# Performance work log

Hardware: AMD Instinct MI355X
Metric: run time of the kernel (lower is better)

The kernel has to match this reference:

```python
import jax, jax.numpy as jnp
import numpy as np

EPS = 1e-12  # F.normalize default eps


def setup_inputs() -> dict:
    key = jax.random.key(0)
    k1, k2, k3, k4 = jax.random.split(key, 4)
    b, n, c, h = 8, 4096, 768, 8
    scale = 1.0 / np.sqrt(c)
    return {
        "x": jax.random.normal(k1, (b, n, c), dtype=jnp.float32),
        "W_qkv": jax.random.normal(k2, (c, 3 * c), dtype=jnp.float32) * scale,
        "W_proj": jax.random.normal(k3, (c, c), dtype=jnp.float32) * scale,
        "b_proj": jax.random.normal(k4, (c,), dtype=jnp.float32) * 0.01,
        "temperature": jnp.ones((h, 1, 1), dtype=jnp.float32),
    }


def _l2norm(t):
    # F.normalize(t, dim=-1): t / max(||t||_2, eps)
    nrm = jnp.sqrt(jnp.sum(t * t, axis=-1, keepdims=True))
    return t / jnp.maximum(nrm, EPS)


def reference(x, W_qkv, W_proj, b_proj, temperature):
    b, n, c = x.shape
    h = temperature.shape[0]
    d = c // h  # head_dim
    # qkv: (b, n, 3c) -> (b, n, 3, h, d) -> (3, b, h, d, n)
    qkv = (x @ W_qkv).reshape(b, n, 3, h, d).transpose(2, 0, 3, 4, 1)
    q, k, v = qkv[0], qkv[1], qkv[2]  # each (b, h, d, n)
    qn = _l2norm(q)
    kn = _l2norm(k)
    # cross-covariance attention: (b, h, d, d)
    attn = jnp.einsum('bhdn,bhen->bhde', qn, kn) * temperature
    attn = jax.nn.softmax(attn, axis=-1)
    out = jnp.einsum('bhde,bhen->bhdn', attn, v)  # (b, h, d, n)
    out = out.transpose(0, 3, 1, 2).reshape(b, n, c)
    return out @ W_proj + b_proj
```

## Files before the change

kernel.cpp:

```cpp
#include <hip/hip_runtime.h>
#include <math.h>

#define NB  8
#define SEQ 4096
#define CH  768
#define NH  8
#define HD  96
#define NC3 2304

typedef _Float16 f16x8 __attribute__((ext_vector_type(8)));
typedef float    f32x4 __attribute__((ext_vector_type(4)));

static const size_t XT_B   = 0;
static const size_t UT_B   = 0;
static const size_t ATT_B  = 28311552;
static const size_t MT_B   = 29491200;
static const size_t PT_B   = 38928384;
static const size_t GP_B   = 50331648;
static const size_t XH_B   = 50331648;
static const size_t WH_B   = 100663296;
static const size_t WT_B   = 104202240;
static const size_t WPT_B  = 107741184;
static const size_t G_B    = 108920832;
static const size_t INV_B  = 118358016;
static const size_t XH2_B  = 118407168;
static const size_t XH_BYTES = (size_t)NB * SEQ * CH * 2;

__device__ __forceinline__ void gload16(const void* g, void* l) {
  __builtin_amdgcn_global_load_lds(
      (const __attribute__((address_space(1))) void*)g,
      (__attribute__((address_space(3))) void*)l, 16, 0, 0);
}

__global__ void cvt_f16_kernel(const float* __restrict__ in,
                               _Float16* __restrict__ out, int n4) {
  int i = blockIdx.x * blockDim.x + threadIdx.x;
  if (i < n4) {
    float4 v = *(const float4*)(in + (size_t)i * 4);
    _Float16* o = out + (size_t)i * 4;
    o[0] = (_Float16)v.x; o[1] = (_Float16)v.y;
    o[2] = (_Float16)v.z; o[3] = (_Float16)v.w;
  }
}

__global__ void transpose_cvt_kernel(const float* __restrict__ in,
                                     _Float16* __restrict__ outT,
                                     _Float16* __restrict__ outH,
                                     int R, int C, long sIn, long sOut) {
  __shared__ float t[32][33];
  const int b = blockIdx.z;
  const int c0 = blockIdx.x * 32, r0 = blockIdx.y * 32;
  const int tx = threadIdx.x & 31, ty = threadIdx.x >> 5;
  const float* ib = in + (size_t)b * sIn;
  _Float16* ob = outT + (size_t)b * sOut;
#pragma unroll
  for (int k = 0; k < 4; ++k) {
    float v = ib[(size_t)(r0 + ty + 8 * k) * C + c0 + tx];
    t[ty + 8 * k][tx] = v;
    if (outH)
      outH[(size_t)b * sOut + (size_t)(r0 + ty + 8 * k) * C + c0 + tx] = (_Float16)v;
  }
  __syncthreads();
#pragma unroll
  for (int k = 0; k < 4; ++k)
    ob[(size_t)(c0 + ty + 8 * k) * R + r0 + tx] = (_Float16)t[tx][ty + 8 * k];
}

template<bool FP16OUT, bool BIAS, bool TRI>
__global__ __launch_bounds__(256) void gemm_bt_mfma(
    const _Float16* __restrict__ Ap, const _Float16* __restrict__ Bp,
    const float* __restrict__ bias, void* __restrict__ Cp,
    int K, int lda, int ldb, int ldc,
    long sA, long sB, long sC, int zdiv, long aCS, long bCS, long cCS,
    int gx, int gy) {
  __shared__ __align__(16) _Float16 ldsA[3][128 * 32];
  __shared__ __align__(16) _Float16 ldsB[3][128 * 32];

  const int nwg = gridDim.x;
  const int lid = blockIdx.x;
  const int wg = (lid & 7) * (nwg >> 3) + (lid >> 3);
  int bx, by, z;
  if constexpr (TRI) {
    int tt = wg % 21; z = wg / 21;
    int ti = 0, rem = tt;
    while (rem >= 6 - ti) { rem -= 6 - ti; ++ti; }
    by = ti; bx = ti + rem;
  } else {
    bx = wg % gx; int r2 = wg / gx; by = r2 % gy; z = r2 / gy;
  }
  const int bat = z % zdiv, chk = z / zdiv;
  const _Float16* A = Ap + (size_t)bat * sA + (size_t)chk * aCS;
  const _Float16* B = Bp + (size_t)bat * sB + (size_t)chk * bCS;
  const size_t cOff = (size_t)bat * sC + (size_t)chk * cCS;

  const int row0 = by * 128, col0 = bx * 128;
  const int tid = threadIdx.x;
  const int l = tid & 63, w = tid >> 6;
  const int lo = l & 15, hi = l >> 4;
  const int wr = w >> 1, wc = w & 1;
  const int rw = 32 * w;
  const int lr = l >> 2;
  const int ls = l & 3;

  f32x4 acc[4][4];
#pragma unroll
  for (int i = 0; i < 4; ++i)
#pragma unroll
    for (int j = 0; j < 4; ++j)
      acc[i][j] = (f32x4){0.f, 0.f, 0.f, 0.f};

  auto STAGE = [&](int hb, int k0) {
#pragma unroll
    for (int q = 0; q < 2; ++q) {
      const int r = rw + 16 * q + lr;
      const int ck = ls ^ ((r >> 1) & 3);
      gload16(A + (size_t)(row0 + r) * lda + k0 + 8 * ck,
              &ldsA[hb][(rw + 16 * q) * 32]);
      gload16(B + (size_t)(col0 + r) * ldb + k0 + 8 * ck,
              &ldsB[hb][(rw + 16 * q) * 32]);
    }
  };

  const int nt = K / 32;
  STAGE(0, 0);
  if (nt > 1) STAGE(1, 32);
  int cur = 0;
  for (int t = 0; t < nt; ++t) {
    if (t + 2 < nt) {
      int n2 = cur + 2; if (n2 >= 3) n2 -= 3;
      STAGE(n2, 32 * (t + 2));
      asm volatile("s_waitcnt vmcnt(8)" ::: "memory");
    } else if (t + 1 < nt) {
      asm volatile("s_waitcnt vmcnt(4)" ::: "memory");
    } else {
      asm volatile("s_waitcnt vmcnt(0)" ::: "memory");
    }
    __builtin_amdgcn_s_barrier();

    f16x8 a[4], b[4];
#pragma unroll
    for (int mi = 0; mi < 4; ++mi) {
      int Ra = 64 * wr + 16 * mi + lo;
      a[mi] = *(const f16x8*)&ldsA[cur][Ra * 32 + (hi ^ ((Ra >> 1) & 3)) * 8];
    }
#pragma unroll
    for (int ni = 0; ni < 4; ++ni) {
      int Rb = 64 * wc + 16 * ni + lo;
      b[ni] = *(const f16x8*)&ldsB[cur][Rb * 32 + (hi ^ ((Rb >> 1) & 3)) * 8];
    }
#pragma unroll
    for (int mi = 0; mi < 4; ++mi)
#pragma unroll
      for (int ni = 0; ni < 4; ++ni)
        acc[mi][ni] = __builtin_amdgcn_mfma_f32_16x16x32_f16(
            a[mi], b[ni], acc[mi][ni], 0, 0, 0);

    __builtin_amdgcn_s_barrier();
    ++cur; if (cur == 3) cur = 0;
  }

#pragma unroll
  for (int ni = 0; ni < 4; ++ni) {
    const int col = col0 + 64 * wc + 16 * ni + lo;
    float bv = 0.f;
    if constexpr (BIAS) bv = bias[col];
#pragma unroll
    for (int mi = 0; mi < 4; ++mi) {
      const int rowb = row0 + 64 * wr + 16 * mi + 4 * hi;
#pragma unroll
      for (int r = 0; r < 4; ++r) {
        float v = acc[mi][ni][r] + bv;
        if constexpr (FP16OUT)
          ((_Float16*)Cp)[cOff + (size_t)(rowb + r) * ldc + col] = (_Float16)v;
        else
          ((float*)Cp)[cOff + (size_t)(rowb + r) * ldc + col] = v;
      }
    }
  }
}

__global__ void reduce_mirror_kernel(const _Float16* __restrict__ GP,
                                     _Float16* __restrict__ G) {
  const int t = blockIdx.x, b = blockIdx.y;
  int ti = 0, rem = t;
  while (rem >= 6 - ti) { rem -= 6 - ti; ++ti; }
  const int tj = ti + rem;
  const int i0 = ti * 128, j0 = tj * 128;
  const int tx = threadIdx.x & 31, ty = threadIdx.x >> 5;
  __shared__ float lds[32][33];
  const size_t cs = (size_t)NB * CH * CH;
  const _Float16* gp = GP + (size_t)b * CH * CH;
  _Float16* g = G + (size_t)b * CH * CH;

  for (int st = 0; st < 16; ++st) {
    const int sr = i0 + (st >> 2) * 32, sc = j0 + (st & 3) * 32;
    __syncthreads();
#pragma unroll
    for (int k = 0; k < 4; ++k) {
      const int r = ty + 8 * k;
      const size_t off = (size_t)(sr + r) * CH + sc + tx;
      float v = ((float)gp[off] + (float)gp[cs + off]) +
                ((float)gp[2 * cs + off] + (float)gp[3 * cs + off]);
      lds[r][tx] = v;
      g[off] = (_Float16)v;
    }
    if (ti != tj) {
      __syncthreads();
#pragma unroll
      for (int k = 0; k < 4; ++k) {
        const int r = ty + 8 * k;
        g[(size_t)(sc + r) * CH + sr + tx] = (_Float16)lds[tx][r];
      }
    }
  }
}

__global__ void norm_kernel(const _Float16* __restrict__ Ut,
                            const _Float16* __restrict__ Wt,
                            float* __restrict__ INVv) {
  const int z = blockIdx.x;
  const int t = z >> 3;
  const int c = blockIdx.y * 128 + threadIdx.x;
  const _Float16* u = Ut + ((size_t)z * CH + c) * CH;
  const _Float16* wv = Wt + ((size_t)(t * CH + c)) * CH;
  float s = 0.f;
  for (int i = 0; i < CH; i += 8) {
    f16x8 uv = *(const f16x8*)(u + i);
    f16x8 wq = *(const f16x8*)(wv + i);
#pragma unroll
    for (int q = 0; q < 8; ++q) s += (float)uv[q] * (float)wq[q];
  }
  s = fmaxf(s, 0.f);
  INVv[(size_t)z * CH + c] = 1.0f / fmaxf(sqrtf(s), 1e-12f);
}

__global__ __launch_bounds__(256) void sattn_kernel(
    const _Float16* __restrict__ WT_, const _Float16* __restrict__ UT_,
    const float* __restrict__ INVv, const float* __restrict__ temp,
    _Float16* __restrict__ ATt) {
  const int bh = blockIdx.x;
  const int b = bh >> 3, h = bh & 7;
  __shared__ __align__(16) _Float16 lds[2][192 * 32];
  __shared__ float S[96][100];

  const int tid = threadIdx.x;
  const int l = tid & 63, w = tid >> 6;
  const int lo = l & 15, hi = l >> 4;
  const int wr = w >> 1, wc = w & 1;
  const int lr = l >> 2, lq = l & 3;

  const _Float16* Abase = WT_ + (size_t)(h * HD) * CH;
  const _Float16* Bbase = UT_ + ((size_t)(8 + b) * CH + h * HD) * CH;

  f32x4 acc[3][3];
#pragma unroll
  for (int i = 0; i < 3; ++i)
#pragma unroll
    for (int j = 0; j < 3; ++j)
      acc[i][j] = (f32x4){0.f, 0.f, 0.f, 0.f};

  auto STAGE = [&](int hb, int k0) {
#pragma unroll
    for (int c = 0; c < 3; ++c) {
      const int group = w * 3 + c;
      const int row = group * 16 + lr;
      const int ck = lq ^ ((row >> 1) & 3);
      const _Float16* src = (row < 96)
          ? Abase + (size_t)row * CH + k0 + 8 * ck
          : Bbase + (size_t)(row - 96) * CH + k0 + 8 * ck;
      gload16(src, &lds[hb][group * 512]);
    }
  };

  STAGE(0, 0);
  int cur = 0;
  for (int t = 0; t < 24; ++t) {
    if (t + 1 < 24) {
      STAGE(cur ^ 1, 32 * (t + 1));
      asm volatile("s_waitcnt vmcnt(3)" ::: "memory");
    } else {
      asm volatile("s_waitcnt vmcnt(0)" ::: "memory");
    }
    __builtin_amdgcn_s_barrier();

    f16x8 a[3], bb[3];
#pragma unroll
    for (int mi = 0; mi < 3; ++mi) {
      const int Ra = 48 * wr + 16 * mi + lo;
      a[mi] = *(const f16x8*)&lds[cur][Ra * 32 + (hi ^ ((Ra >> 1) & 3)) * 8];
    }
#pragma unroll
    for (int ni = 0; ni < 3; ++ni) {
      const int Rb = 96 + 48 * wc + 16 * ni + lo;
      bb[ni] = *(const f16x8*)&lds[cur][Rb * 32 + (hi ^ ((Rb >> 1) & 3)) * 8];
    }
#pragma unroll
    for (int mi = 0; mi < 3; ++mi)
#pragma unroll
      for (int ni = 0; ni < 3; ++ni)
        acc[mi][ni] = __builtin_amdgcn_mfma_f32_16x16x32_f16(
            a[mi], bb[ni], acc[mi][ni], 0, 0, 0);

    __builtin_amdgcn_s_barrier();
    cur ^= 1;
  }

  const float tv = temp[h];
  const float* iq = INVv + (size_t)b * CH + h * HD;
  const float* ik = INVv + (size_t)(8 + b) * CH + h * HD;
#pragma unroll
  for (int ni = 0; ni < 3; ++ni) {
    const int col = 48 * wc + 16 * ni + lo;
    const float ikv = ik[col];
#pragma unroll
    for (int mi = 0; mi < 3; ++mi) {
      const int rb = 48 * wr + 16 * mi + 4 * hi;
#pragma unroll
      for (int r = 0; r < 4; ++r)
        S[rb + r][col] = acc[mi][ni][r] * iq[rb + r] * ikv * tv;
    }
  }
  __syncthreads();

  const int g16 = tid >> 4, l16 = tid & 15;
  _Float16* ab = ATt + (size_t)bh * 9216;
#pragma unroll
  for (int it = 0; it < 6; ++it) {
    const int d = g16 + 16 * it;
    float v[6];
    float mx = -INFINITY;
#pragma unroll
    for (int j = 0; j < 6; ++j) { v[j] = S[d][l16 * 6 + j]; mx = fmaxf(mx, v[j]); }
#pragma unroll
    for (int m = 1; m < 16; m <<= 1) mx = fmaxf(mx, __shfl_xor(mx, m, 16));
    float sum = 0.f;
#pragma unroll
    for (int j = 0; j < 6; ++j) { v[j] = __expf(v[j] - mx); sum += v[j]; }
#pragma unroll
    for (int m = 1; m < 16; m <<= 1) sum += __shfl_xor(sum, m, 16);
    const float inv = 1.0f / sum;
#pragma unroll
    for (int j = 0; j < 6; ++j)
      ab[(size_t)(l16 * 6 + j) * 96 + d] = (_Float16)(v[j] * inv);
  }
}

__global__ void mt_kernel(const _Float16* __restrict__ Wpt,
                          const _Float16* __restrict__ ATt,
                          _Float16* __restrict__ Mt) {
  const int j0 = blockIdx.x * 128;
  const int bh = blockIdx.y;
  const int b = bh >> 3, h = bh & 7;
  const int tx = threadIdx.x & 15, ty = threadIdx.x >> 4;
  __shared__ float Ws[16][128], Ats[16][96];
  float acc[8][6] = {};

  for (int d0 = 0; d0 < 96; d0 += 16) {
    {
      int jj = threadIdx.x >> 1, s8 = (threadIdx.x & 1) * 8;
      f16x8 v = *(const f16x8*)(Wpt + (size_t)(j0 + jj) * CH + h * HD + d0 + s8);
#pragma unroll
      for (int q = 0; q < 8; ++q) Ws[s8 + q][jj] = (float)v[q];
    }
    if (threadIdx.x < 192) {
      int e = threadIdx.x >> 1, s8 = (threadIdx.x & 1) * 8;
      f16x8 v = *(const f16x8*)(ATt + (size_t)bh * 9216 + (size_t)e * 96 + d0 + s8);
#pragma unroll
      for (int q = 0; q < 8; ++q) Ats[s8 + q][e] = (float)v[q];
    }
    __syncthreads();
#pragma unroll
    for (int kk = 0; kk < 16; ++kk) {
      float a[8], bb[6];
#pragma unroll
      for (int i = 0; i < 8; ++i) a[i] = Ws[kk][ty * 8 + i];
#pragma unroll
      for (int j = 0; j < 6; ++j) bb[j] = Ats[kk][tx * 6 + j];
#pragma unroll
      for (int i = 0; i < 8; ++i)
#pragma unroll
        for (int j = 0; j < 6; ++j)
          acc[i][j] += a[i] * bb[j];
    }
    __syncthreads();
  }

  _Float16* mb = Mt + (size_t)b * CH * CH;
#pragma unroll
  for (int i = 0; i < 8; ++i)
#pragma unroll
    for (int j = 0; j < 6; ++j)
      mb[(size_t)(j0 + ty * 8 + i) * CH + h * HD + tx * 6 + j] = (_Float16)acc[i][j];
}

extern "C" void kernel_launch(void* const* d_in, const int* in_sizes, int n_in,
                              void* d_out, int out_size, void* d_ws, size_t ws_size,
                              hipStream_t stream) {
  const float* x      = (const float*)d_in[0];
  const float* W_qkv  = (const float*)d_in[1];
  const float* W_proj = (const float*)d_in[2];
  const float* b_proj = (const float*)d_in[3];
  const float* temp   = (const float*)d_in[4];
  float* out = (float*)d_out;
  char* ws = (char*)d_ws;

  _Float16* XT  = (_Float16*)(ws + XT_B);
  _Float16* UT  = (_Float16*)(ws + UT_B);
  _Float16* ATT = (_Float16*)(ws + ATT_B);
  _Float16* MT  = (_Float16*)(ws + MT_B);
  _Float16* PT  = (_Float16*)(ws + PT_B);
  _Float16* GP  = (_Float16*)(ws + GP_B);
  _Float16* XH  = (_Float16*)(ws + XH_B);
  _Float16* WH  = (_Float16*)(ws + WH_B);
  _Float16* WT  = (_Float16*)(ws + WT_B);
  _Float16* WPT = (_Float16*)(ws + WPT_B);
  _Float16* G   = (_Float16*)(ws + G_B);
  float*    INV = (float*)   (ws + INV_B);

  const bool fast = ws_size >= XH2_B + XH_BYTES;
  _Float16* XHU = fast ? (_Float16*)(ws + XH2_B) : XH;

  const long CC = (long)CH * CH;
  const long SC = (long)SEQ * CH;

  cvt_f16_kernel<<<(CH * NC3 / 4 + 255) / 256, 256, 0, stream>>>(
      W_qkv, WH, CH * NC3 / 4);
  transpose_cvt_kernel<<<dim3(CH / 32, SEQ / 32, NB), 256, 0, stream>>>(
      x, XT, fast ? XHU : nullptr, SEQ, CH, SC, SC);
  transpose_cvt_kernel<<<dim3(NC3 / 32, CH / 32, 1), 256, 0, stream>>>(
      W_qkv, WT, nullptr, CH, NC3, 0, 0);
  transpose_cvt_kernel<<<dim3(CH / 32, CH / 32, 1), 256, 0, stream>>>(
      W_proj, WPT, nullptr, CH, CH, 0, 0);

  gemm_bt_mfma<true, false, true><<<672, 256, 0, stream>>>(
      XT, XT, nullptr, GP, 1024, SEQ, SEQ, CH,
      (long)CH * SEQ, (long)CH * SEQ, CC, NB, 1024, 1024, (long)NB * CC,
      21, 1);

  reduce_mirror_kernel<<<dim3(21, NB), 256, 0, stream>>>(GP, G);

  gemm_bt_mfma<true, false, false><<<576, 256, 0, stream>>>(
      WT, G, nullptr, UT, CH, CH, CH, CH,
      0, CC, CC, NB, CC, 0, (long)NB * CC, 6, 6);

  norm_kernel<<<dim3(16, 6), 128, 0, stream>>>(UT, WT, INV);

  sattn_kernel<<<64, 256, 0, stream>>>(WT, UT, INV, temp, ATT);

  mt_kernel<<<dim3(6, 64), 256, 0, stream>>>(WPT, ATT, MT);

  gemm_bt_mfma<true, false, false><<<288, 256, 0, stream>>>(
      MT, WH + 2 * CH, nullptr, PT, CH, CH, NC3, CH,
      CC, 0, CC, NB, 0, 0, 0, 6, 6);

  if (!fast)
    cvt_f16_kernel<<<(int)(NB * SC / 4 / 256), 256, 0, stream>>>(
        x, XH, (int)(NB * SC / 4));

  gemm_bt_mfma<false, true, false><<<1536, 256, 0, stream>>>(
      XHU, PT, b_proj, out, CH, CH, CH, CH,
      SC, CC, SC, NB, 0, 0, 0, 6, 32);
}
```

Before: 266.9 us.

## Vectorize transpose kernels, fuse W_qkv conversion, stage fp32 GEMM epilogue through LDS

```diff
diff --git a/kernel.cpp b/kernel.cpp
--- a/kernel.cpp
+++ b/kernel.cpp
@@ -9,6 +9,7 @@
 #define NC3 2304
 
 typedef _Float16 f16x8 __attribute__((ext_vector_type(8)));
+typedef _Float16 f16x4 __attribute__((ext_vector_type(4)));
 typedef float    f32x4 __attribute__((ext_vector_type(4)));
 
 static const size_t XT_B   = 0;
@@ -43,27 +44,39 @@
   }
 }
 
-__global__ void transpose_cvt_kernel(const float* __restrict__ in,
-                                     _Float16* __restrict__ outT,
-                                     _Float16* __restrict__ outH,
-                                     int R, int C, long sIn, long sOut) {
-  __shared__ float t[32][33];
+__global__ __launch_bounds__(256) void transpose64_kernel(
+    const float* __restrict__ in, _Float16* __restrict__ outT,
+    _Float16* __restrict__ outH, int R, int C, long sIn, long sOut) {
+  __shared__ __align__(16) float ts[64][68];
   const int b = blockIdx.z;
-  const int c0 = blockIdx.x * 32, r0 = blockIdx.y * 32;
-  const int tx = threadIdx.x & 31, ty = threadIdx.x >> 5;
+  const int c0 = blockIdx.x * 64, r0 = blockIdx.y * 64;
   const float* ib = in + (size_t)b * sIn;
-  _Float16* ob = outT + (size_t)b * sOut;
-#pragma unroll
-  for (int k = 0; k < 4; ++k) {
-    float v = ib[(size_t)(r0 + ty + 8 * k) * C + c0 + tx];
-    t[ty + 8 * k][tx] = v;
-    if (outH)
-      outH[(size_t)b * sOut + (size_t)(r0 + ty + 8 * k) * C + c0 + tx] = (_Float16)v;
+
+  const int c4 = (threadIdx.x & 15) * 4;
+  const int rr = threadIdx.x >> 4;
+#pragma unroll
+  for (int q = 0; q < 4; ++q) {
+    const int row = rr + 16 * q;
+    float4 v = *(const float4*)&ib[(size_t)(r0 + row) * C + c0 + c4];
+    *(float4*)&ts[row][c4] = v;
+    if (outH) {
+      f16x4 h = {(_Float16)v.x, (_Float16)v.y, (_Float16)v.z, (_Float16)v.w};
+      *(f16x4*)&outH[(size_t)b * sOut + (size_t)(r0 + row) * C + c0 + c4] = h;
+    }
   }
   __syncthreads();
-#pragma unroll
-  for (int k = 0; k < 4; ++k)
-    ob[(size_t)(c0 + ty + 8 * k) * R + r0 + tx] = (_Float16)t[tx][ty + 8 * k];
+
+  const int col = threadIdx.x >> 2;
+  const int nseg = (threadIdx.x & 3) * 16;
+  _Float16* ob = outT + (size_t)b * sOut + (size_t)(c0 + col) * R + r0 + nseg;
+#pragma unroll
+  for (int half = 0; half < 2; ++half) {
+    f16x8 h;
+#pragma unroll
+    for (int j = 0; j < 8; ++j)
+      h[j] = (_Float16)ts[nseg + half * 8 + j][col];
+    *(f16x8*)&ob[half * 8] = h;
+  }
 }
 
 template<bool FP16OUT, bool BIAS, bool TRI>
@@ -159,21 +172,41 @@
     ++cur; if (cur == 3) cur = 0;
   }
 
-#pragma unroll
-  for (int ni = 0; ni < 4; ++ni) {
-    const int col = col0 + 64 * wc + 16 * ni + lo;
-    float bv = 0.f;
-    if constexpr (BIAS) bv = bias[col];
+  if constexpr (!FP16OUT) {
+    float* smw = (float*)&ldsA[0][0] + w * 1088;
+    float* Cb = (float*)Cp + cOff;
+    float bv[4];
+#pragma unroll
+    for (int ni = 0; ni < 4; ++ni)
+      bv[ni] = BIAS ? bias[col0 + 64 * wc + 16 * ni + lo] : 0.f;
+    const int grow = l & 15, gseg = l >> 4;
 #pragma unroll
     for (int mi = 0; mi < 4; ++mi) {
-      const int rowb = row0 + 64 * wr + 16 * mi + 4 * hi;
-#pragma unroll
-      for (int r = 0; r < 4; ++r) {
-        float v = acc[mi][ni][r] + bv;
-        if constexpr (FP16OUT)
-          ((_Float16*)Cp)[cOff + (size_t)(rowb + r) * ldc + col] = (_Float16)v;
-        else
-          ((float*)Cp)[cOff + (size_t)(rowb + r) * ldc + col] = v;
+#pragma unroll
+      for (int ni = 0; ni < 4; ++ni)
+#pragma unroll
+        for (int r = 0; r < 4; ++r)
+          smw[(4 * hi + r) * 68 + 16 * ni + lo] = acc[mi][ni][r] + bv[ni];
+#pragma unroll
+      for (int j = 0; j < 4; ++j) {
+        float4 v = *(const float4*)&smw[grow * 68 + gseg * 16 + 4 * j];
+        *(float4*)&Cb[(size_t)(row0 + 64 * wr + 16 * mi + grow) * ldc
+                      + col0 + 64 * wc + gseg * 16 + 4 * j] = v;
+      }
+    }
+  } else {
+#pragma unroll
+    for (int ni = 0; ni < 4; ++ni) {
+      const int col = col0 + 64 * wc + 16 * ni + lo;
+      float bv = 0.f;
+      if constexpr (BIAS) bv = bias[col];
+#pragma unroll
+      for (int mi = 0; mi < 4; ++mi) {
+        const int rowb = row0 + 64 * wr + 16 * mi + 4 * hi;
+#pragma unroll
+        for (int r = 0; r < 4; ++r)
+          ((_Float16*)Cp)[cOff + (size_t)(rowb + r) * ldc + col] =
+              (_Float16)(acc[mi][ni][r] + bv);
       }
     }
   }
@@ -423,13 +456,11 @@
   const long CC = (long)CH * CH;
   const long SC = (long)SEQ * CH;
 
-  cvt_f16_kernel<<<(CH * NC3 / 4 + 255) / 256, 256, 0, stream>>>(
-      W_qkv, WH, CH * NC3 / 4);
-  transpose_cvt_kernel<<<dim3(CH / 32, SEQ / 32, NB), 256, 0, stream>>>(
+  transpose64_kernel<<<dim3(CH / 64, SEQ / 64, NB), 256, 0, stream>>>(
       x, XT, fast ? XHU : nullptr, SEQ, CH, SC, SC);
-  transpose_cvt_kernel<<<dim3(NC3 / 32, CH / 32, 1), 256, 0, stream>>>(
-      W_qkv, WT, nullptr, CH, NC3, 0, 0);
-  transpose_cvt_kernel<<<dim3(CH / 32, CH / 32, 1), 256, 0, stream>>>(
+  transpose64_kernel<<<dim3(NC3 / 64, CH / 64, 1), 256, 0, stream>>>(
+      W_qkv, WT, WH, CH, NC3, 0, 0);
+  transpose64_kernel<<<dim3(CH / 64, CH / 64, 1), 256, 0, stream>>>(
       W_proj, WPT, nullptr, CH, CH, 0, 0);
 
   gemm_bt_mfma<true, false, true><<<672, 256, 0, stream>>>(
```

Measured after the change: 265.4 us. No clear change (-0.6%).
